# Kernel tuning notes

Measured on AMD Instinct MI355X. Metric: run time of the kernel, lower is better.

The kernel has to match this reference:

```python
import math
import jax, jax.numpy as jnp
import numpy as np

NUM_HEADS = 16
ROTARY_BASE = 10000.0
FMIN = -3.4028234663852886e+38  # torch uses -FLT_MAX as the blocked logit value


def setup_inputs() -> dict:
    key = jax.random.key(0)
    ks = jax.random.split(key, 4)
    B, S, D = 2, 2048, 2048
    x = jax.random.normal(ks[0], (B, S, D), dtype=jnp.float32)
    mask = jnp.ones((B, S), dtype=bool)
    # Linear params stored as [in, out] (transpose of torch's [out, in])
    w_in = jax.random.normal(ks[1], (D, 3 * D), dtype=jnp.float32) * 0.02
    b_in = jnp.zeros((3 * D,), dtype=jnp.float32)
    w_out = jax.random.normal(ks[2], (D, D), dtype=jnp.float32) * 0.02
    b_out = jnp.zeros((D,), dtype=jnp.float32)
    return {"x": x, "mask": mask, "w_in": w_in, "b_in": b_in,
            "w_out": w_out, "b_out": b_out}


def _rotate_half(t):
    # curated-transformers RotaryEmbeddings._rotate: [-x2, x1]
    h = t.shape[-1] // 2
    return jnp.concatenate([-t[..., h:], t[..., :h]], axis=-1)


def _rope_cos_sin(seq_len, width):
    # theta_i = base^(-2i/d); m_theta duplicated (rotate-half / NeoX layout)
    theta = ROTARY_BASE ** (-jnp.arange(0, width, 2, dtype=jnp.float32) / width)
    m_theta = jnp.arange(seq_len, dtype=jnp.float32)[:, None] * theta[None, :]
    m_theta = jnp.concatenate([m_theta, m_theta], axis=-1)  # [S, width]
    return jnp.cos(m_theta), jnp.sin(m_theta)


def reference(x, mask, w_in, b_in, w_out, b_out):
    B, S, D = x.shape
    H = NUM_HEADS
    Dh = D // H

    proj = x @ w_in + b_in                       # [B, S, 3D]
    q, k, v = jnp.split(proj, 3, axis=-1)
    split = lambda t: t.reshape(B, S, H, Dh).transpose(0, 2, 1, 3)  # [B,H,S,Dh]
    q, k, v = split(q), split(k), split(v)

    # rotary_fraction == 1.0 -> full-head rotary, default positions 0..S-1
    cos, sin = _rope_cos_sin(S, Dh)              # [S, Dh]
    cos = cos[None, None]
    sin = sin[None, None]
    q = cos * q + sin * _rotate_half(q)
    k = cos * k + sin * _rotate_half(k)

    scores = jnp.einsum('bhqd,bhkd->bhqk', q, k) / math.sqrt(Dh)
    # causal mask (use_causal_mask=True): strictly upper triangle blocked
    causal = jnp.triu(jnp.full((S, S), FMIN, dtype=scores.dtype), k=1)
    scores = scores + causal[None, None]
    # padding mask: (1 - mask) * -FLT_MAX, broadcast over heads and queries
    logit_mask = (1.0 - mask.astype(scores.dtype)) * FMIN
    scores = scores + logit_mask[:, None, None, :]

    attn_w = jax.nn.softmax(scores, axis=-1)
    attn = jnp.einsum('bhqk,bhkd->bhqd', attn_w, v)  # dropout_prob=0 (eval)
    attn = attn.transpose(0, 2, 1, 3).reshape(B, S, D)  # combine_heads
    return attn @ w_out + b_out
```

## Files before the change

kernel.cpp:

```cpp
#include <hip/hip_runtime.h>

typedef unsigned short ushort_t;
typedef unsigned int u32;
typedef short bf16x8 __attribute__((ext_vector_type(8)));
typedef float f32x4 __attribute__((ext_vector_type(4)));

__device__ __forceinline__ ushort_t f2bf(float f) {
  u32 u = __float_as_uint(f);
  u += 0x7FFFu + ((u >> 16) & 1u);
  return (ushort_t)(u >> 16);
}
__device__ __forceinline__ float bf2f(ushort_t h) {
  return __uint_as_float(((u32)h) << 16);
}

__device__ __forceinline__ void async_cp16(const void* g, void* l) {
  __builtin_amdgcn_global_load_lds(
      (const u32 __attribute__((address_space(1)))*)(unsigned long long)g,
      (u32 __attribute__((address_space(3)))*)(u32)(unsigned long long)l,
      16, 0, 0);
}

#define MFMA_BF16(a, b, c) __builtin_amdgcn_mfma_f32_16x16x32_bf16((a), (b), (c), 0, 0, 0)

#define KFENCE() __asm__ __volatile__("" ::: "memory")
#define KBAR()                    \
  do {                            \
    KFENCE();                     \
    __builtin_amdgcn_s_barrier(); \
    KFENCE();                     \
  } while (0)

__global__ void cvt_bf16_k(const float* __restrict__ in, ushort_t* __restrict__ out, int n4) {
  int i = blockIdx.x * blockDim.x + threadIdx.x;
  if (i >= n4) return;
  float4 v = ((const float4*)in)[i];
  unsigned long long p = (unsigned long long)f2bf(v.x)
                       | ((unsigned long long)f2bf(v.y) << 16)
                       | ((unsigned long long)f2bf(v.z) << 32)
                       | ((unsigned long long)f2bf(v.w) << 48);
  ((unsigned long long*)out)[i] = p;
}

__global__ void transpose_cvt_k(const float* __restrict__ in, ushort_t* __restrict__ out,
                                int R, int C) {
  __shared__ float t[32][33];
  int c0 = blockIdx.x * 32, r0 = blockIdx.y * 32;
  int tx = threadIdx.x, ty = threadIdx.y;
#pragma unroll
  for (int i = 0; i < 4; ++i)
    t[ty + i * 8][tx] = in[(size_t)(r0 + ty + i * 8) * C + c0 + tx];
  __syncthreads();
#pragma unroll
  for (int i = 0; i < 4; ++i)
    out[(size_t)(c0 + ty + i * 8) * R + r0 + tx] = f2bf(t[tx][ty + i * 8]);
}

__global__ void rope_swz_k(const ushort_t* __restrict__ q, const ushort_t* __restrict__ k,
                           ushort_t* __restrict__ qs, ushort_t* __restrict__ ks) {
  int row = blockIdx.x * 2 + (threadIdx.x >> 7);
  int d = threadIdx.x & 127;
  int s = row & 2047;
  int i = d & 63;
  float theta = __expf(-(float)i * 0.14391156831212876f);
  float mt = (float)s * theta;
  float sn, cs;
  sincosf(mt, &sn, &cs);
  size_t base = (size_t)row * 128;
  float qd = bf2f(q[base + d]), qp = bf2f(q[base + (d ^ 64)]);
  float kd = bf2f(k[base + d]), kp = bf2f(k[base + (d ^ 64)]);
  float rq = (d < 64) ? -qp : qp;
  float rk = (d < 64) ? -kp : kp;
  size_t bhb = (size_t)(row >> 11) * 262144;
  size_t qoff = bhb + (size_t)((s >> 5) * 4096 + ((d >> 5) * 2 + ((s >> 4) & 1)) * 512 +
                               (((d >> 3) & 3) * 16 + (s & 15)) * 8 + (d & 7));
  size_t koff = bhb + (size_t)((s >> 6) * 8192 + (d >> 5) * 2048 + ((s >> 4) & 3) * 512 +
                               ((d >> 3) & 3) * 128 + (s & 15) * 8 + (d & 7));
  const float scale2 = 0.08838834764831845f * 1.44269504088896340f;
  qs[qoff] = f2bf(scale2 * (cs * qd + sn * rq));
  ks[koff] = f2bf(cs * kd + sn * rk);
}

__device__ __forceinline__ void stage_chunks(const ushort_t* gs, ushort_t* lbase,
                                             int w, int K, int k0, int nchunk) {
  ushort_t* l = lbase + w * 512;
  if (nchunk == 2) {
#pragma unroll
    for (int c = 0; c < 2; ++c)
      async_cp16(gs + (size_t)(c * 64) * K + k0, l + c * 4096);
  } else {
#pragma unroll
    for (int c = 0; c < 4; ++c)
      async_cp16(gs + (size_t)(c * 64) * K + k0, l + c * 4096);
  }
}

template <int MODE>
__global__ __launch_bounds__(512) void gemm_dp_k(
    const ushort_t* __restrict__ A, const ushort_t* __restrict__ Bt,
    const float* __restrict__ bias, float* __restrict__ Cout,
    ushort_t* __restrict__ Qd, ushort_t* __restrict__ Kd, ushort_t* __restrict__ Vd,
    int M, int N, int K) {
  __shared__ ushort_t As[3][8192];
  __shared__ ushort_t Bs[3][16384];

  const int tid = threadIdx.x;
  const int w = tid >> 6, lane = tid & 63;
  const int quad = lane >> 4, l15 = lane & 15;
  const int wr = w >> 2, wc = w & 3;
  const int m0 = blockIdx.y * 128, n0 = blockIdx.x * 256;

  const int rr = (w << 3) + (lane >> 3);
  const int sw = ((lane & 7) ^ ((lane >> 3) & 7)) << 3;
  const ushort_t* Ags = A + (size_t)(m0 + rr) * K + sw;
  const ushort_t* Bgs = Bt + (size_t)(n0 + rr) * K + sw;

  f32x4 acc[4][4] = {};

  ushort_t *A0 = As[0], *A1 = As[1], *A2 = As[2];
  ushort_t *B0 = Bs[0], *B1 = Bs[1], *B2 = Bs[2];

  stage_chunks(Ags, A0, w, K, 0, 2);
  stage_chunks(Bgs, B0, w, K, 0, 4);
  stage_chunks(Ags, A1, w, K, 64, 2);
  stage_chunks(Bgs, B1, w, K, 64, 4);
  __asm__ __volatile__("s_waitcnt vmcnt(6)" ::: "memory");
  KBAR();

  const int NT = K >> 6;

  for (int t = 0; t < NT; ++t) {
    const bool pre = (t + 2) < NT;
    const int kpre = (t + 2) << 6;

    bf16x8 a[4][2], b0[2][2], b1[2][2];

#pragma unroll
    for (int mt = 0; mt < 4; ++mt)
#pragma unroll
      for (int kk = 0; kk < 2; ++kk) {
        int row = wr * 64 + mt * 16 + l15;
        int gr = ((kk << 2) | quad) ^ (l15 & 7);
        a[mt][kk] = *(const bf16x8*)(A0 + row * 64 + gr * 8);
      }
#pragma unroll
    for (int n2 = 0; n2 < 2; ++n2)
#pragma unroll
      for (int kk = 0; kk < 2; ++kk) {
        int row = wc * 64 + n2 * 16 + l15;
        int gr = ((kk << 2) | quad) ^ (l15 & 7);
        b0[n2][kk] = *(const bf16x8*)(B0 + row * 64 + gr * 8);
      }
    if (pre) {
      stage_chunks(Ags, A2, w, K, kpre, 2);
      stage_chunks(Bgs, B2, w, K, kpre, 4);
    }
    KBAR();
    __builtin_amdgcn_s_setprio(1);
#pragma unroll
    for (int mt = 0; mt < 4; ++mt)
#pragma unroll
      for (int n2 = 0; n2 < 2; ++n2)
#pragma unroll
        for (int kk = 0; kk < 2; ++kk)
          acc[mt][n2] = MFMA_BF16(a[mt][kk], b0[n2][kk], acc[mt][n2]);
    __builtin_amdgcn_s_setprio(0);
    KBAR();

#pragma unroll
    for (int n2 = 0; n2 < 2; ++n2)
#pragma unroll
      for (int kk = 0; kk < 2; ++kk) {
        int row = wc * 64 + 32 + n2 * 16 + l15;
        int gr = ((kk << 2) | quad) ^ (l15 & 7);
        b1[n2][kk] = *(const bf16x8*)(B0 + row * 64 + gr * 8);
      }
    KBAR();
    __builtin_amdgcn_s_setprio(1);
#pragma unroll
    for (int mt = 0; mt < 4; ++mt)
#pragma unroll
      for (int n2 = 0; n2 < 2; ++n2)
#pragma unroll
        for (int kk = 0; kk < 2; ++kk)
          acc[mt][2 + n2] = MFMA_BF16(a[mt][kk], b1[n2][kk], acc[mt][2 + n2]);
    __builtin_amdgcn_s_setprio(0);
    if (pre) {
      __asm__ __volatile__("s_waitcnt vmcnt(6)" ::: "memory");
    } else {
      __asm__ __volatile__("s_waitcnt vmcnt(0)" ::: "memory");
    }
    KBAR();
    ushort_t* tA = A0; A0 = A1; A1 = A2; A2 = tA;
    ushort_t* tB = B0; B0 = B1; B1 = B2; B2 = tB;
  }

  if (MODE == 0) {
#pragma unroll
    for (int mt = 0; mt < 4; ++mt)
#pragma unroll
      for (int nt = 0; nt < 4; ++nt) {
        int col = n0 + wc * 64 + nt * 16 + l15;
        float bv = bias[col];
#pragma unroll
        for (int r = 0; r < 4; ++r) {
          int row = m0 + wr * 64 + mt * 16 + quad * 4 + r;
          Cout[(size_t)row * N + col] = acc[mt][nt][r] + bv;
        }
      }
  } else {
#pragma unroll
    for (int mt = 0; mt < 4; ++mt)
#pragma unroll
      for (int nt = 0; nt < 4; ++nt) {
        int col = n0 + wc * 64 + nt * 16 + l15;
        int which = col >> 11;
        int rem = col & 2047;
        int h = rem >> 7, d = rem & 127;
        float bv = bias[col];
#pragma unroll
        for (int r = 0; r < 4; ++r) {
          int row = m0 + wr * 64 + mt * 16 + quad * 4 + r;
          int bb = row >> 11, s = row & 2047;
          size_t bhb = (size_t)(bb * 16 + h) * 262144;
          ushort_t val = f2bf(acc[mt][nt][r] + bv);
          if (which == 2) {
            size_t off = bhb + (size_t)((s >> 6) * 8192 + ((s >> 5) & 1) * 4096 +
                                        (d >> 4) * 512 + ((s >> 3) & 3) * 128 +
                                        (d & 15) * 8 + (s & 7));
            Vd[off] = val;
          } else {
            ushort_t* dst = (which == 0) ? Qd : Kd;
            dst[bhb + (size_t)s * 128 + d] = val;
          }
        }
      }
  }
}

__global__ __launch_bounds__(64, 3) void attn_flash_k(
    const ushort_t* __restrict__ Qs, const ushort_t* __restrict__ Ks,
    const ushort_t* __restrict__ Vs, ushort_t* __restrict__ Ob) {
  __shared__ ushort_t Pw[1024];

  const int lane = threadIdx.x & 63;
  const int quad = lane >> 4, l15 = lane & 15;
  const int n = blockIdx.x;
  const int bh = (n & 7) * 4 + ((n >> 3) & 3);
  const int sx = n >> 5;
  const int g = (sx & 1) ? (sx >> 1) : (127 - (sx >> 1));
  const int b = bh >> 4, h = bh & 15;
  const int q0 = g * 16;
  const int ktmax = g >> 2;
  const int G = g >> 1, mt = g & 1;
  const size_t bhb = (size_t)bh * 262144;

  bf16x8 qa[4];
#pragma unroll
  for (int kq = 0; kq < 4; ++kq)
    qa[kq] = *(const bf16x8*)(Qs + bhb + G * 4096 + (kq * 2 + mt) * 512 + lane * 8);

  f32x4 o[8] = {};
  float mi[4], li[4];
#pragma unroll
  for (int r = 0; r < 4; ++r) { mi[r] = -1e30f; li[r] = 0.f; }

  for (int kt = 0; kt <= ktmax; ++kt) {
    const int k0 = kt * 64;
    const ushort_t* kbase = Ks + bhb + (size_t)kt * 8192;
    const ushort_t* vbase = Vs + bhb + (size_t)kt * 8192;

    f32x4 sa[4] = {};
#pragma unroll
    for (int h2 = 0; h2 < 2; ++h2) {
      bf16x8 kb2[2][4];
#pragma unroll
      for (int kq = 0; kq < 2; ++kq)
#pragma unroll
        for (int nt = 0; nt < 4; ++nt)
          kb2[kq][nt] =
              *(const bf16x8*)(kbase + ((h2 * 2 + kq) * 4 + nt) * 512 + lane * 8);
#pragma unroll
      for (int kq = 0; kq < 2; ++kq)
#pragma unroll
        for (int nt = 0; nt < 4; ++nt)
          sa[nt] = MFMA_BF16(qa[h2 * 2 + kq], kb2[kq][nt], sa[nt]);
    }

    bf16x8 vb0[8];
#pragma unroll
    for (int nt = 0; nt < 8; ++nt)
      vb0[nt] = *(const bf16x8*)(vbase + nt * 512 + lane * 8);

    const bool diag = (kt == ktmax);
#pragma unroll
    for (int r = 0; r < 4; ++r) {
      int qg = q0 + quad * 4 + r;
      float sv[4];
      float rmax = -1e30f;
#pragma unroll
      for (int nt = 0; nt < 4; ++nt) {
        float vv = sa[nt][r];
        if (diag) { int kgc = k0 + nt * 16 + l15; if (kgc > qg) vv = -1e30f; }
        sv[nt] = vv;
        rmax = fmaxf(rmax, vv);
      }
      rmax = fmaxf(rmax, __shfl_xor(rmax, 1));
      rmax = fmaxf(rmax, __shfl_xor(rmax, 2));
      rmax = fmaxf(rmax, __shfl_xor(rmax, 4));
      rmax = fmaxf(rmax, __shfl_xor(rmax, 8));
      float mnew = fmaxf(mi[r], rmax);
      float alpha = exp2f(mi[r] - mnew);
      float psum = 0.f;
#pragma unroll
      for (int nt = 0; nt < 4; ++nt) {
        float p = exp2f(sv[nt] - mnew);
        psum += p;
        Pw[(nt >> 1) * 512 + (nt & 1) * 256 + (l15 >> 3) * 128 +
           quad * 32 + r * 8 + (l15 & 7)] = f2bf(p);
      }
      psum += __shfl_xor(psum, 1);
      psum += __shfl_xor(psum, 2);
      psum += __shfl_xor(psum, 4);
      psum += __shfl_xor(psum, 8);
      li[r] = li[r] * alpha + psum;
      mi[r] = mnew;
#pragma unroll
      for (int nt = 0; nt < 8; ++nt) o[nt][r] *= alpha;
    }

    __asm__ __volatile__("" ::: "memory");

    {
      bf16x8 pa = *(const bf16x8*)(Pw + lane * 8);
#pragma unroll
      for (int nt = 0; nt < 8; ++nt)
        o[nt] = MFMA_BF16(pa, vb0[nt], o[nt]);
    }
    {
      bf16x8 vb1[8];
#pragma unroll
      for (int nt = 0; nt < 8; ++nt)
        vb1[nt] = *(const bf16x8*)(vbase + (8 + nt) * 512 + lane * 8);
      bf16x8 pa = *(const bf16x8*)(Pw + 512 + lane * 8);
#pragma unroll
      for (int nt = 0; nt < 8; ++nt)
        o[nt] = MFMA_BF16(pa, vb1[nt], o[nt]);
    }
  }

#pragma unroll
  for (int r = 0; r < 4; ++r) {
    float inv = 1.f / li[r];
    int s = q0 + quad * 4 + r;
    size_t rowbase = ((size_t)b * 2048 + s) * 2048 + h * 128;
#pragma unroll
    for (int nt = 0; nt < 8; ++nt)
      Ob[rowbase + nt * 16 + l15] = f2bf(o[nt][r] * inv);
  }
}

extern "C" void kernel_launch(void* const* d_in, const int* in_sizes, int n_in,
                              void* d_out, int out_size, void* d_ws, size_t ws_size,
                              hipStream_t stream) {
  const float* x     = (const float*)d_in[0];
  const float* w_in  = (const float*)d_in[2];
  const float* b_in  = (const float*)d_in[3];
  const float* w_out = (const float*)d_in[4];
  const float* b_out = (const float*)d_in[5];
  float* out = (float*)d_out;

  ushort_t* x_bf    = (ushort_t*)d_ws;
  ushort_t* w_in_t  = x_bf + 8388608;
  ushort_t* w_out_t = w_in_t + 12582912;
  ushort_t* q       = w_out_t + 4194304;
  ushort_t* k       = q + 8388608;
  ushort_t* vswz    = k + 8388608;

  ushort_t* qswz = x_bf;
  ushort_t* kswz = w_in_t;
  ushort_t* attn = q;

  cvt_bf16_k<<<dim3(8192), dim3(256), 0, stream>>>(x, x_bf, 2097152);
  transpose_cvt_k<<<dim3(192, 64), dim3(32, 8), 0, stream>>>(w_in, w_in_t, 2048, 6144);
  transpose_cvt_k<<<dim3(64, 64), dim3(32, 8), 0, stream>>>(w_out, w_out_t, 2048, 2048);
  gemm_dp_k<1><<<dim3(24, 32), dim3(512), 0, stream>>>(
      x_bf, w_in_t, b_in, nullptr, q, k, vswz, 4096, 6144, 2048);
  rope_swz_k<<<dim3(32768), dim3(256), 0, stream>>>(q, k, qswz, kswz);
  attn_flash_k<<<dim3(4096), dim3(64), 0, stream>>>(qswz, kswz, vswz, attn);
  gemm_dp_k<0><<<dim3(8, 32), dim3(512), 0, stream>>>(
      attn, w_out_t, b_out, out, nullptr, nullptr, nullptr, 4096, 2048, 2048);
}
```

Measured before the change: 427.6 us.

## Fuse RoPE and Q/K swizzle into the QKV GEMM epilogue

The separate rope_swz kernel is removed. RoPE, the softmax scale and the swizzled Q/K layout writes now happen in the QKV projection GEMM epilogue. To put each rotate-half pair in adjacent lanes, the w_in transpose permutes the Q/K output columns, so the partner value comes from a shuffle-xor by 1. This drops an extra kernel launch and a full read and write of Q and K, at the cost of per-element sincos work and scattered stores in the GEMM epilogue.

```diff
diff --git a/kernel.cpp b/kernel.cpp
--- a/kernel.cpp
+++ b/kernel.cpp
@@ -43,7 +43,7 @@
 }
 
 __global__ void transpose_cvt_k(const float* __restrict__ in, ushort_t* __restrict__ out,
-                                int R, int C) {
+                                int R, int C, int perm) {
   __shared__ float t[32][33];
   int c0 = blockIdx.x * 32, r0 = blockIdx.y * 32;
   int tx = threadIdx.x, ty = threadIdx.y;
@@ -52,33 +52,15 @@
     t[ty + i * 8][tx] = in[(size_t)(r0 + ty + i * 8) * C + c0 + tx];
   __syncthreads();
 #pragma unroll
-  for (int i = 0; i < 4; ++i)
-    out[(size_t)(c0 + ty + i * 8) * R + r0 + tx] = f2bf(t[tx][ty + i * 8]);
-}
-
-__global__ void rope_swz_k(const ushort_t* __restrict__ q, const ushort_t* __restrict__ k,
-                           ushort_t* __restrict__ qs, ushort_t* __restrict__ ks) {
-  int row = blockIdx.x * 2 + (threadIdx.x >> 7);
-  int d = threadIdx.x & 127;
-  int s = row & 2047;
-  int i = d & 63;
-  float theta = __expf(-(float)i * 0.14391156831212876f);
-  float mt = (float)s * theta;
-  float sn, cs;
-  sincosf(mt, &sn, &cs);
-  size_t base = (size_t)row * 128;
-  float qd = bf2f(q[base + d]), qp = bf2f(q[base + (d ^ 64)]);
-  float kd = bf2f(k[base + d]), kp = bf2f(k[base + (d ^ 64)]);
-  float rq = (d < 64) ? -qp : qp;
-  float rk = (d < 64) ? -kp : kp;
-  size_t bhb = (size_t)(row >> 11) * 262144;
-  size_t qoff = bhb + (size_t)((s >> 5) * 4096 + ((d >> 5) * 2 + ((s >> 4) & 1)) * 512 +
-                               (((d >> 3) & 3) * 16 + (s & 15)) * 8 + (d & 7));
-  size_t koff = bhb + (size_t)((s >> 6) * 8192 + (d >> 5) * 2048 + ((s >> 4) & 3) * 512 +
-                               ((d >> 3) & 3) * 128 + (s & 15) * 8 + (d & 7));
-  const float scale2 = 0.08838834764831845f * 1.44269504088896340f;
-  qs[qoff] = f2bf(scale2 * (cs * qd + sn * rq));
-  ks[koff] = f2bf(cs * kd + sn * rk);
+  for (int i = 0; i < 4; ++i) {
+    int cc = c0 + ty + i * 8;
+    int oc = cc;
+    if (perm && cc < 4096) {
+      int p = cc & 127;
+      oc = (cc & ~127) | ((p & 63) << 1) | (p >> 6);
+    }
+    out[(size_t)oc * R + r0 + tx] = f2bf(t[tx][ty + i * 8]);
+  }
 }
 
 __device__ __forceinline__ void stage_chunks(const ushort_t* gs, ushort_t* lbase,
@@ -209,32 +191,61 @@
         }
       }
   } else {
-#pragma unroll
-    for (int mt = 0; mt < 4; ++mt)
-#pragma unroll
-      for (int nt = 0; nt < 4; ++nt) {
-        int col = n0 + wc * 64 + nt * 16 + l15;
-        int which = col >> 11;
-        int rem = col & 2047;
-        int h = rem >> 7, d = rem & 127;
+    const float scale2 = 0.08838834764831845f * 1.44269504088896340f;
+#pragma unroll
+    for (int nt = 0; nt < 4; ++nt) {
+      int col = n0 + wc * 64 + nt * 16 + l15;
+      int which = col >> 11;
+      int rem = col & 2047;
+      int h = rem >> 7;
+      if (which == 2) {
+        int d = rem & 127;
         float bv = bias[col];
 #pragma unroll
-        for (int r = 0; r < 4; ++r) {
-          int row = m0 + wr * 64 + mt * 16 + quad * 4 + r;
-          int bb = row >> 11, s = row & 2047;
-          size_t bhb = (size_t)(bb * 16 + h) * 262144;
-          ushort_t val = f2bf(acc[mt][nt][r] + bv);
-          if (which == 2) {
+        for (int mt = 0; mt < 4; ++mt)
+#pragma unroll
+          for (int r = 0; r < 4; ++r) {
+            int row = m0 + wr * 64 + mt * 16 + quad * 4 + r;
+            int bb = row >> 11, s = row & 2047;
+            size_t bhb = (size_t)(bb * 16 + h) * 262144;
             size_t off = bhb + (size_t)((s >> 6) * 8192 + ((s >> 5) & 1) * 4096 +
                                         (d >> 4) * 512 + ((s >> 3) & 3) * 128 +
                                         (d & 15) * 8 + (s & 7));
-            Vd[off] = val;
-          } else {
-            ushort_t* dst = (which == 0) ? Qd : Kd;
-            dst[bhb + (size_t)s * 128 + d] = val;
+            Vd[off] = f2bf(acc[mt][nt][r] + bv);
           }
-        }
-      }
+      } else {
+        int dp = rem & 127;
+        int i2 = dp >> 1;
+        int d = i2 + ((dp & 1) << 6);
+        float bv = bias[(col & ~127) | d];
+        float theta = __expf(-(float)i2 * 0.14391156831212876f);
+        float sgn = (dp & 1) ? 1.f : -1.f;
+#pragma unroll
+        for (int mt = 0; mt < 4; ++mt)
+#pragma unroll
+          for (int r = 0; r < 4; ++r) {
+            int row = m0 + wr * 64 + mt * 16 + quad * 4 + r;
+            int bb = row >> 11, s = row & 2047;
+            float val = acc[mt][nt][r] + bv;
+            float vp = __shfl_xor(val, 1);
+            float sn, cs;
+            sincosf((float)s * theta, &sn, &cs);
+            float ov = cs * val + sn * sgn * vp;
+            size_t bhb = (size_t)(bb * 16 + h) * 262144;
+            if (which == 0) {
+              size_t off = bhb + (size_t)((s >> 5) * 4096 +
+                           ((d >> 5) * 2 + ((s >> 4) & 1)) * 512 +
+                           (((d >> 3) & 3) * 16 + (s & 15)) * 8 + (d & 7));
+              Qd[off] = f2bf(scale2 * ov);
+            } else {
+              size_t off = bhb + (size_t)((s >> 6) * 8192 + (d >> 5) * 2048 +
+                           ((s >> 4) & 3) * 512 + ((d >> 3) & 3) * 128 +
+                           (s & 15) * 8 + (d & 7));
+              Kd[off] = f2bf(ov);
+            }
+          }
+      }
+    }
   }
 }
 
@@ -373,20 +384,16 @@
   ushort_t* x_bf    = (ushort_t*)d_ws;
   ushort_t* w_in_t  = x_bf + 8388608;
   ushort_t* w_out_t = w_in_t + 12582912;
-  ushort_t* q       = w_out_t + 4194304;
-  ushort_t* k       = q + 8388608;
-  ushort_t* vswz    = k + 8388608;
-
-  ushort_t* qswz = x_bf;
-  ushort_t* kswz = w_in_t;
-  ushort_t* attn = q;
+  ushort_t* qswz    = w_out_t + 4194304;
+  ushort_t* kswz    = qswz + 8388608;
+  ushort_t* vswz    = kswz + 8388608;
+  ushort_t* attn    = x_bf;
 
   cvt_bf16_k<<<dim3(8192), dim3(256), 0, stream>>>(x, x_bf, 2097152);
-  transpose_cvt_k<<<dim3(192, 64), dim3(32, 8), 0, stream>>>(w_in, w_in_t, 2048, 6144);
-  transpose_cvt_k<<<dim3(64, 64), dim3(32, 8), 0, stream>>>(w_out, w_out_t, 2048, 2048);
+  transpose_cvt_k<<<dim3(192, 64), dim3(32, 8), 0, stream>>>(w_in, w_in_t, 2048, 6144, 1);
+  transpose_cvt_k<<<dim3(64, 64), dim3(32, 8), 0, stream>>>(w_out, w_out_t, 2048, 2048, 0);
   gemm_dp_k<1><<<dim3(24, 32), dim3(512), 0, stream>>>(
-      x_bf, w_in_t, b_in, nullptr, q, k, vswz, 4096, 6144, 2048);
-  rope_swz_k<<<dim3(32768), dim3(256), 0, stream>>>(q, k, qswz, kswz);
+      x_bf, w_in_t, b_in, nullptr, qswz, kswz, vswz, 4096, 6144, 2048);
   attn_flash_k<<<dim3(4096), dim3(64), 0, stream>>>(qswz, kswz, vswz, attn);
   gemm_dp_k<0><<<dim3(8, 32), dim3(512), 0, stream>>>(
       attn, w_out_t, b_out, out, nullptr, nullptr, nullptr, 4096, 2048, 2048);
```

Result: slower. 452.4 us (+5.8%).
